# Kernel tuning notes

Measured on AMD Instinct MI355X. Metric: run time of the kernel, lower is better.

Reference implementation:

```python
import jax, jax.numpy as jnp
import numpy as np

B, T, DIM = 8, 2048, 512
DM, EXPAND, NSTATE, HDIM, L = 128, 2, 16, 64, 2
DINNER = DM * EXPAND            # 256
NH = DINNER // HDIM             # 4 heads
CONVDIM = DINNER + 2 * NSTATE   # 288 (n_groups=1)
PROJ = DINNER + CONVDIM + NH    # 548
K = 4                           # conv kernel (HF default)
EPS = 1e-5


def setup_inputs() -> dict:
    key = jax.random.key(0)
    ks = jax.random.split(key, 8)
    s = 0.02
    return {
        "x": jax.random.normal(ks[0], (B, T, DIM), jnp.float32),
        "in_w": jax.random.normal(ks[1], (DIM, DM), jnp.float32) * s,
        "in_b": jnp.zeros((DM,), jnp.float32),
        "norm_w": jnp.ones((L, DM), jnp.float32),
        "inproj_w": jax.random.normal(ks[2], (L, DM, PROJ), jnp.float32) * s,
        "conv_w": jax.random.normal(ks[3], (L, CONVDIM, 1, K), jnp.float32) * 0.2,
        "conv_b": jnp.zeros((L, CONVDIM), jnp.float32),
        "A_log": jnp.log(jax.random.uniform(ks[4], (L, NH), jnp.float32, 1.0, 8.0)),
        "D": jnp.ones((L, NH), jnp.float32),
        "dt_bias": jnp.log(jnp.expm1(jax.random.uniform(ks[5], (L, NH), jnp.float32, 1e-3, 0.1))),
        "gnorm_w": jnp.ones((L, DINNER), jnp.float32),
        "outproj_w": jax.random.normal(ks[6], (L, DINNER, DM), jnp.float32) * s,
        "normf_w": jnp.ones((DM,), jnp.float32),
        "out_w": jax.random.normal(ks[7], (DM, DIM), jnp.float32) * s,
        "out_b": jnp.zeros((DIM,), jnp.float32),
    }


def _rmsnorm(x, w):
    var = jnp.mean(x * x, axis=-1, keepdims=True)
    return x * jax.lax.rsqrt(var + EPS) * w


def _gated_rmsnorm(y, gate, w):
    y = y * jax.nn.silu(gate)
    var = jnp.mean(y * y, axis=-1, keepdims=True)
    return y * jax.lax.rsqrt(var + EPS) * w


def _causal_conv(h, w, b):
    # h: [B,T,C] depthwise causal conv, kernel K, left pad K-1
    out = jax.lax.conv_general_dilated(
        h.swapaxes(1, 2), w, (1,), [(K - 1, 0)],
        feature_group_count=CONVDIM,
        dimension_numbers=("NCH", "OIH", "NCH"))
    return out.swapaxes(1, 2) + b


def _ssd(xs, dt, A, Bm, Cm, Dh):
    # selective state-space scan (math-equivalent to HF Mamba2 chunked SSD)
    # xs [B,T,H,P], dt [B,T,H], A [H], Bm/Cm [B,T,N], Dh [H]
    dA = jnp.exp(dt * A)  # [B,T,H]

    def step(state, inp):
        dA_t, dt_t, x_t, B_t, C_t = inp
        dBx = dt_t[:, :, None, None] * x_t[..., None] * B_t[:, None, None, :]
        state = state * dA_t[:, :, None, None] + dBx  # [B,H,P,N]
        y = jnp.einsum("bhpn,bn->bhp", state, C_t)
        return state, y

    init = jnp.zeros((xs.shape[0], NH, HDIM, NSTATE), xs.dtype)
    _, ys = jax.lax.scan(step, init, (dA.swapaxes(0, 1), dt.swapaxes(0, 1),
                                      xs.swapaxes(0, 1), Bm.swapaxes(0, 1), Cm.swapaxes(0, 1)))
    return ys.swapaxes(0, 1) + xs * Dh[None, None, :, None]


def reference(x, in_w, in_b, norm_w, inproj_w, conv_w, conv_b, A_log, D,
              dt_bias, gnorm_w, outproj_w, normf_w, out_w, out_b):
    h = x @ in_w + in_b  # [B,T,DM]
    for l in range(L):
        res = h
        hn = _rmsnorm(h, norm_w[l])
        proj = hn @ inproj_w[l]  # [B,T,PROJ]
        gate = proj[..., :DINNER]
        hBC = proj[..., DINNER:DINNER + CONVDIM]
        dt = proj[..., DINNER + CONVDIM:]
        hBC = jax.nn.silu(_causal_conv(hBC, conv_w[l], conv_b[l]))
        xs = hBC[..., :DINNER].reshape(B, T, NH, HDIM)
        Bm = hBC[..., DINNER:DINNER + NSTATE]
        Cm = hBC[..., DINNER + NSTATE:]
        A = -jnp.exp(A_log[l])
        dt = jax.nn.softplus(dt + dt_bias[l])  # time_step_limit=(0,inf): no clamp
        y = _ssd(xs, dt, A, Bm, Cm, D[l]).reshape(B, T, DINNER)
        y = _gated_rmsnorm(y, gate, gnorm_w[l])
        h = res + y @ outproj_w[l]
    h = _rmsnorm(h, normf_w)
    pooled = h.mean(axis=1)  # mean pool over T
    return pooled @ out_w + out_b
```

## Files before the change

### kernel.cpp

```cpp
#include <hip/hip_runtime.h>
#include <math.h>

typedef unsigned short ushort_t;
typedef unsigned int uint_t;

#define B_      8
#define T_      2048
#define DIMX    512
#define DM      128
#define DINNER  256
#define NSTATE  16
#define HDIM    64
#define NH      4
#define CONVDIM 288
#define PROJ    548
#define KCONV   4
#define LLAYERS 2
#define QCH     128
#define NC      (T_/QCH)
#define EPSF    1e-5f
#define MTOK    (B_*T_)

#define OFF_H      0u
#define OFF_DTP    19988480u
#define OFF_CUM    20054016u
#define OFF_Z      20119552u
#define OFF_DEC    21168128u
#define OFF_PART   21168640u
#define OFF_WTIN   23396864u
#define OFF_WTINP  23429632u
#define OFF_WTOUT  23503360u
#define OFF_PROJB  23600000u
#define OFF_DTRAW  28100000u
#define OFF_HBCB   28200000u
#define OFF_YB     30600000u

__device__ __forceinline__ ushort_t f2b(float f) {
    uint_t u = __builtin_bit_cast(uint_t, f);
    return (ushort_t)((u + 0x7FFFu + ((u >> 16) & 1u)) >> 16);
}
__device__ __forceinline__ float b2f(ushort_t b) {
    uint_t u = ((uint_t)b) << 16;
    return __builtin_bit_cast(float, u);
}
__device__ __forceinline__ float blo(uint_t u) { return b2f((ushort_t)(u & 0xffffu)); }
__device__ __forceinline__ float bhi(uint_t u) { return b2f((ushort_t)(u >> 16)); }

typedef short bf8 __attribute__((ext_vector_type(8)));
typedef float f4v __attribute__((ext_vector_type(4)));

__global__ __launch_bounds__(256) void k_wt_all(
    const float* __restrict__ in_w, const float* __restrict__ inproj_w,
    const float* __restrict__ outproj_w,
    ushort_t* __restrict__ wt_in, ushort_t* __restrict__ wt_inp,
    ushort_t* __restrict__ wt_out)
{
    __shared__ float tile[64][65];
    int idx = blockIdx.x;
    const float* W; ushort_t* Wt; int K, N, k0, n0;
    if (idx < 16) {
        W = in_w; Wt = wt_in; K = 512; N = 128;
        k0 = (idx & 7) * 64; n0 = (idx >> 3) * 64;
    } else if (idx < 52) {
        int r = idx - 16; int l = r / 18; r -= l * 18;
        W = inproj_w + l * 128 * PROJ; Wt = wt_inp + l * 576 * 128; K = 128; N = PROJ;
        k0 = (r & 1) * 64; n0 = (r >> 1) * 64;
    } else {
        int r = idx - 52; int l = r / 8; r -= l * 8;
        W = outproj_w + l * 256 * 128; Wt = wt_out + l * 128 * 256; K = 256; N = 128;
        k0 = (r & 3) * 64; n0 = (r >> 2) * 64;
    }
    const int tid = threadIdx.x;
#pragma unroll
    for (int it = 0; it < 16; ++it) {
        const int e = it * 256 + tid;
        const int kk = e >> 6, nn = e & 63;
        tile[kk][nn] = (n0 + nn < N) ? W[(k0 + kk) * N + (n0 + nn)] : 0.f;
    }
    __syncthreads();
#pragma unroll
    for (int it = 0; it < 16; ++it) {
        const int e = it * 256 + tid;
        const int nn = e >> 6, kk = e & 63;
        Wt[(n0 + nn) * K + k0 + kk] = f2b(tile[kk][nn]);
    }
}

template<int KTOT, int LDC, int NGUARD, int EPI, bool ABF16>
__global__ __launch_bounds__(256) void k_gemm(
    const void* __restrict__ Ap, const ushort_t* __restrict__ Bt,
    const float* __restrict__ aux, float* __restrict__ C)
{
    __shared__ ushort_t Als[64 * 136];
    __shared__ ushort_t Bls[64 * 136];
    const int m0 = blockIdx.x * 64, n0 = blockIdx.y * 64;
    const int tid = threadIdx.x;
    const int lane = tid & 63, w = tid >> 6;
    const int wm = (w >> 1) * 32, wn = (w & 1) * 32;
    const int r16 = lane & 15, q8 = (lane >> 4) * 8;

    f4v acc[2][2];
#pragma unroll
    for (int i = 0; i < 2; ++i)
#pragma unroll
        for (int j = 0; j < 2; ++j) acc[i][j] = (f4v)0.f;

    for (int kc = 0; kc < KTOT; kc += 128) {
        if constexpr (ABF16) {
            const ushort_t* A = (const ushort_t*)Ap;
#pragma unroll
            for (int i = 0; i < 4; ++i) {
                const int e = i * 2048 + tid * 8;
                const int r = e >> 7, c = e & 127;
                *(uint4*)&Als[r * 136 + c] = *(const uint4*)&A[(m0 + r) * KTOT + kc + c];
            }
        } else {
            const float* A = (const float*)Ap;
#pragma unroll
            for (int i = 0; i < 4; ++i) {
                const int e = i * 2048 + tid * 8;
                const int r = e >> 7, c = e & 127;
                const float4 f0 = *(const float4*)&A[(m0 + r) * KTOT + kc + c];
                const float4 f1 = *(const float4*)&A[(m0 + r) * KTOT + kc + c + 4];
                uint4 pk;
                pk.x = (uint_t)f2b(f0.x) | ((uint_t)f2b(f0.y) << 16);
                pk.y = (uint_t)f2b(f0.z) | ((uint_t)f2b(f0.w) << 16);
                pk.z = (uint_t)f2b(f1.x) | ((uint_t)f2b(f1.y) << 16);
                pk.w = (uint_t)f2b(f1.z) | ((uint_t)f2b(f1.w) << 16);
                *(uint4*)&Als[r * 136 + c] = pk;
            }
        }
#pragma unroll
        for (int i = 0; i < 4; ++i) {
            const int e = i * 2048 + tid * 8;
            const int r = e >> 7, c = e & 127;
            *(uint4*)&Bls[r * 136 + c] = *(const uint4*)&Bt[(n0 + r) * KTOT + kc + c];
        }
        __syncthreads();
#pragma unroll
        for (int kk = 0; kk < 128; kk += 32) {
            const bf8 a0 = *(const bf8*)&Als[(wm + r16) * 136 + kk + q8];
            const bf8 a1 = *(const bf8*)&Als[(wm + 16 + r16) * 136 + kk + q8];
            const bf8 b0 = *(const bf8*)&Bls[(wn + r16) * 136 + kk + q8];
            const bf8 b1 = *(const bf8*)&Bls[(wn + 16 + r16) * 136 + kk + q8];
            acc[0][0] = __builtin_amdgcn_mfma_f32_16x16x32_bf16(a0, b0, acc[0][0], 0, 0, 0);
            acc[0][1] = __builtin_amdgcn_mfma_f32_16x16x32_bf16(a0, b1, acc[0][1], 0, 0, 0);
            acc[1][0] = __builtin_amdgcn_mfma_f32_16x16x32_bf16(a1, b0, acc[1][0], 0, 0, 0);
            acc[1][1] = __builtin_amdgcn_mfma_f32_16x16x32_bf16(a1, b1, acc[1][1], 0, 0, 0);
        }
        __syncthreads();
    }
    const int q4 = (lane >> 4) * 4;
#pragma unroll
    for (int i = 0; i < 2; ++i)
#pragma unroll
        for (int j = 0; j < 2; ++j)
#pragma unroll
            for (int r = 0; r < 4; ++r) {
                const int grow = m0 + wm + i * 16 + q4 + r;
                const int gcol = n0 + wn + j * 16 + r16;
                if (NGUARD == 0 || gcol < NGUARD) {
                    float v = acc[i][j][r];
                    if (EPI == 1) v += aux[gcol];
                    if (EPI == 2) v += C[grow * LDC + gcol];
                    C[grow * LDC + gcol] = v;
                }
            }
}

__global__ __launch_bounds__(256) void k_gemm_rms(
    const float* __restrict__ h, const float* __restrict__ nw,
    const ushort_t* __restrict__ Bt, ushort_t* __restrict__ projb,
    float* __restrict__ dtraw)
{
    __shared__ ushort_t Als[64 * 136];
    __shared__ ushort_t Bls[64 * 136];
    const int m0 = blockIdx.x * 64, n0 = blockIdx.y * 64;
    const int tid = threadIdx.x;
    const int lane = tid & 63, w = tid >> 6;
    const int wm = (w >> 1) * 32, wn = (w & 1) * 32;
    const int r16 = lane & 15, q8 = (lane >> 4) * 8;

#pragma unroll
    for (int i = 0; i < 4; ++i) {
        const int e = i * 2048 + tid * 8;
        const int r = e >> 7, c = e & 127;
        const float4 f0 = *(const float4*)&h[(m0 + r) * 128 + c];
        const float4 f1 = *(const float4*)&h[(m0 + r) * 128 + c + 4];
        float ss = f0.x * f0.x + f0.y * f0.y + f0.z * f0.z + f0.w * f0.w
                 + f1.x * f1.x + f1.y * f1.y + f1.z * f1.z + f1.w * f1.w;
#pragma unroll
        for (int off = 1; off < 16; off <<= 1) ss += __shfl_xor(ss, off);
        const float rs = rsqrtf(ss * (1.f / 128.f) + EPSF);
        const float4 w0 = *(const float4*)&nw[c];
        const float4 w1 = *(const float4*)&nw[c + 4];
        uint4 pk;
        pk.x = (uint_t)f2b(f0.x * rs * w0.x) | ((uint_t)f2b(f0.y * rs * w0.y) << 16);
        pk.y = (uint_t)f2b(f0.z * rs * w0.z) | ((uint_t)f2b(f0.w * rs * w0.w) << 16);
        pk.z = (uint_t)f2b(f1.x * rs * w1.x) | ((uint_t)f2b(f1.y * rs * w1.y) << 16);
        pk.w = (uint_t)f2b(f1.z * rs * w1.z) | ((uint_t)f2b(f1.w * rs * w1.w) << 16);
        *(uint4*)&Als[r * 136 + c] = pk;
    }
#pragma unroll
    for (int i = 0; i < 4; ++i) {
        const int e = i * 2048 + tid * 8;
        const int r = e >> 7, c = e & 127;
        *(uint4*)&Bls[r * 136 + c] = *(const uint4*)&Bt[(n0 + r) * 128 + c];
    }
    __syncthreads();

    f4v acc[2][2];
#pragma unroll
    for (int i = 0; i < 2; ++i)
#pragma unroll
        for (int j = 0; j < 2; ++j) acc[i][j] = (f4v)0.f;
#pragma unroll
    for (int kk = 0; kk < 128; kk += 32) {
        const bf8 a0 = *(const bf8*)&Als[(wm + r16) * 136 + kk + q8];
        const bf8 a1 = *(const bf8*)&Als[(wm + 16 + r16) * 136 + kk + q8];
        const bf8 b0 = *(const bf8*)&Bls[(wn + r16) * 136 + kk + q8];
        const bf8 b1 = *(const bf8*)&Bls[(wn + 16 + r16) * 136 + kk + q8];
        acc[0][0] = __builtin_amdgcn_mfma_f32_16x16x32_bf16(a0, b0, acc[0][0], 0, 0, 0);
        acc[0][1] = __builtin_amdgcn_mfma_f32_16x16x32_bf16(a0, b1, acc[0][1], 0, 0, 0);
        acc[1][0] = __builtin_amdgcn_mfma_f32_16x16x32_bf16(a1, b0, acc[1][0], 0, 0, 0);
        acc[1][1] = __builtin_amdgcn_mfma_f32_16x16x32_bf16(a1, b1, acc[1][1], 0, 0, 0);
    }

    const int q4 = (lane >> 4) * 4;
#pragma unroll
    for (int i = 0; i < 2; ++i)
#pragma unroll
        for (int j = 0; j < 2; ++j)
#pragma unroll
            for (int r = 0; r < 4; ++r) {
                const int grow = m0 + wm + i * 16 + q4 + r;
                const int gcol = n0 + wn + j * 16 + r16;
                if (gcol < 544) projb[grow * 544 + gcol] = f2b(acc[i][j][r]);
                else if (gcol < PROJ) dtraw[grow * 4 + (gcol - 544)] = acc[i][j][r];
            }
}

__global__ __launch_bounds__(256) void k_gemm_gn(
    const ushort_t* __restrict__ yb, const ushort_t* __restrict__ projb,
    const float* __restrict__ gw, const ushort_t* __restrict__ Bt,
    float* __restrict__ C)
{
    __shared__ ushort_t Als[64 * 264];
    __shared__ ushort_t Bls[64 * 136];
    const int m0 = blockIdx.x * 64, n0 = blockIdx.y * 64;
    const int tid = threadIdx.x;
    const int lane = tid & 63, w = tid >> 6;
    const int wm = (w >> 1) * 32, wn = (w & 1) * 32;
    const int r16 = lane & 15, q8 = (lane >> 4) * 8;

#pragma unroll
    for (int i = 0; i < 8; ++i) {
        const int e = i * 2048 + tid * 8;
        const int r = e >> 8, c = e & 255;
        const uint4 yv = *(const uint4*)&yb[(m0 + r) * 256 + c];
        const uint4 gv = *(const uint4*)&projb[(m0 + r) * 544 + c];
        const float g0 = blo(gv.x), g1 = bhi(gv.x), g2 = blo(gv.y), g3 = bhi(gv.y);
        const float g4 = blo(gv.z), g5 = bhi(gv.z), g6 = blo(gv.w), g7 = bhi(gv.w);
        float v0 = blo(yv.x) * (g0 / (1.f + __expf(-g0)));
        float v1 = bhi(yv.x) * (g1 / (1.f + __expf(-g1)));
        float v2 = blo(yv.y) * (g2 / (1.f + __expf(-g2)));
        float v3 = bhi(yv.y) * (g3 / (1.f + __expf(-g3)));
        float v4 = blo(yv.z) * (g4 / (1.f + __expf(-g4)));
        float v5 = bhi(yv.z) * (g5 / (1.f + __expf(-g5)));
        float v6 = blo(yv.w) * (g6 / (1.f + __expf(-g6)));
        float v7 = bhi(yv.w) * (g7 / (1.f + __expf(-g7)));
        float ss = v0 * v0 + v1 * v1 + v2 * v2 + v3 * v3
                 + v4 * v4 + v5 * v5 + v6 * v6 + v7 * v7;
#pragma unroll
        for (int off = 1; off < 32; off <<= 1) ss += __shfl_xor(ss, off);
        const float rs = rsqrtf(ss * (1.f / 256.f) + EPSF);
        const float4 w0 = *(const float4*)&gw[c];
        const float4 w1 = *(const float4*)&gw[c + 4];
        uint4 pk;
        pk.x = (uint_t)f2b(v0 * rs * w0.x) | ((uint_t)f2b(v1 * rs * w0.y) << 16);
        pk.y = (uint_t)f2b(v2 * rs * w0.z) | ((uint_t)f2b(v3 * rs * w0.w) << 16);
        pk.z = (uint_t)f2b(v4 * rs * w1.x) | ((uint_t)f2b(v5 * rs * w1.y) << 16);
        pk.w = (uint_t)f2b(v6 * rs * w1.z) | ((uint_t)f2b(v7 * rs * w1.w) << 16);
        *(uint4*)&Als[r * 264 + c] = pk;
    }

    f4v acc[2][2];
#pragma unroll
    for (int i = 0; i < 2; ++i)
#pragma unroll
        for (int j = 0; j < 2; ++j) acc[i][j] = (f4v)0.f;

    for (int kc = 0; kc < 256; kc += 128) {
#pragma unroll
        for (int i = 0; i < 4; ++i) {
            const int e = i * 2048 + tid * 8;
            const int r = e >> 7, c = e & 127;
            *(uint4*)&Bls[r * 136 + c] = *(const uint4*)&Bt[(n0 + r) * 256 + kc + c];
        }
        __syncthreads();
#pragma unroll
        for (int kk = 0; kk < 128; kk += 32) {
            const bf8 a0 = *(const bf8*)&Als[(wm + r16) * 264 + kc + kk + q8];
            const bf8 a1 = *(const bf8*)&Als[(wm + 16 + r16) * 264 + kc + kk + q8];
            const bf8 b0 = *(const bf8*)&Bls[(wn + r16) * 136 + kk + q8];
            const bf8 b1 = *(const bf8*)&Bls[(wn + 16 + r16) * 136 + kk + q8];
            acc[0][0] = __builtin_amdgcn_mfma_f32_16x16x32_bf16(a0, b0, acc[0][0], 0, 0, 0);
            acc[0][1] = __builtin_amdgcn_mfma_f32_16x16x32_bf16(a0, b1, acc[0][1], 0, 0, 0);
            acc[1][0] = __builtin_amdgcn_mfma_f32_16x16x32_bf16(a1, b0, acc[1][0], 0, 0, 0);
            acc[1][1] = __builtin_amdgcn_mfma_f32_16x16x32_bf16(a1, b1, acc[1][1], 0, 0, 0);
        }
        __syncthreads();
    }

    const int q4 = (lane >> 4) * 4;
#pragma unroll
    for (int i = 0; i < 2; ++i)
#pragma unroll
        for (int j = 0; j < 2; ++j)
#pragma unroll
            for (int r = 0; r < 4; ++r) {
                const int grow = m0 + wm + i * 16 + q4 + r;
                const int gcol = n0 + wn + j * 16 + r16;
                C[grow * 128 + gcol] += acc[i][j][r];
            }
}

__global__ __launch_bounds__(256) void k_convdt(
    const ushort_t* __restrict__ projb, const float* __restrict__ dtraw,
    const float* __restrict__ cw, const float* __restrict__ cb,
    const float* __restrict__ A_log, const float* __restrict__ dt_bias,
    ushort_t* __restrict__ hbcb, float* __restrict__ dtp,
    float* __restrict__ cum, int l)
{
    __shared__ float sc[128];
    const int bid = blockIdx.x;
    const int tid = threadIdx.x;
    if (bid < (MTOK * CONVDIM) / 256) {
        const int e = bid * 256 + tid;
        const int m = e / CONVDIM;
        const int cch = e - m * CONVDIM;
        const int b = m >> 11;
        const int t = m & (T_ - 1);
        const float* wp = cw + (l * CONVDIM + cch) * KCONV;
        float acc = cb[l * CONVDIM + cch];
#pragma unroll
        for (int k = 0; k < KCONV; ++k) {
            const int tt = t - (KCONV - 1) + k;
            if (tt >= 0) acc += b2f(projb[(b * T_ + tt) * 544 + 256 + cch]) * wp[k];
        }
        hbcb[m * CONVDIM + cch] = f2b(acc / (1.f + __expf(-acc)));
    } else {
        const int bid2 = bid - (MTOK * CONVDIM) / 256;
        const int c = bid2 & (NC - 1);
        const int hh = (bid2 / NC) & (NH - 1);
        const int b = bid2 / (NC * NH);
        const int t = tid;
        float dtv = 0.f;
        if (t < 128) {
            const int m = b * T_ + c * QCH + t;
            const float Ah = -expf(A_log[l * NH + hh]);
            const float raw = dtraw[m * 4 + hh] + dt_bias[l * NH + hh];
            dtv = (raw > 20.f) ? raw : log1pf(expf(raw));
            sc[t] = dtv * Ah;
        }
        __syncthreads();
        for (int off = 1; off < 128; off <<= 1) {
            const float v = (t >= off && t < 128) ? sc[t - off] : 0.f;
            __syncthreads();
            if (t < 128) sc[t] += v;
            __syncthreads();
        }
        if (t < 128) {
            const int m = b * T_ + c * QCH + t;
            dtp[m * NH + hh] = dtv;
            cum[m * NH + hh] = sc[t];
        }
    }
}

__global__ __launch_bounds__(256) void k_ssd_state(
    const ushort_t* __restrict__ hbcb, const float* __restrict__ dtp,
    const float* __restrict__ cum, float* __restrict__ zbuf,
    float* __restrict__ dec)
{
    __shared__ ushort_t Xt[64 * 136];
    __shared__ ushort_t wB[16 * 136];
    __shared__ float cumls[QCH];
    __shared__ float dtls[QCH];
    const int bid = blockIdx.x;
    const int c = bid & (NC - 1);
    const int hh = (bid / NC) & (NH - 1);
    const int b = bid / (NC * NH);
    const int m0 = b * T_ + c * QCH;
    const int tid = threadIdx.x;

    if (tid < QCH) {
        cumls[tid] = cum[(m0 + tid) * NH + hh];
        dtls[tid] = dtp[(m0 + tid) * NH + hh];
    }
    __syncthreads();
    const float clast = cumls[QCH - 1];
    {
        const int p = tid & 63;
        const int s0 = tid >> 6;
#pragma unroll
        for (int pass = 0; pass < 32; ++pass) {
            const int s = s0 + pass * 4;
            Xt[p * 136 + s] = hbcb[(m0 + s) * CONVDIM + hh * 64 + p];
        }
    }
    for (int e = tid; e < QCH * 16; e += 256) {
        const int n = e & 15, s = e >> 4;
        const float w = __expf(clast - cumls[s]) * dtls[s];
        wB[n * 136 + s] = f2b(w * b2f(hbcb[(m0 + s) * CONVDIM + DINNER + n]));
    }
    __syncthreads();

    const int lane = tid & 63, w = tid >> 6;
    const int r16 = lane & 15, q8 = (lane >> 4) * 8, q4 = (lane >> 4) * 4;
    f4v acc = (f4v)0.f;
#pragma unroll
    for (int kc = 0; kc < 128; kc += 32) {
        const bf8 a = *(const bf8*)&Xt[(w * 16 + r16) * 136 + kc + q8];
        const bf8 bb = *(const bf8*)&wB[r16 * 136 + kc + q8];
        acc = __builtin_amdgcn_mfma_f32_16x16x32_bf16(a, bb, acc, 0, 0, 0);
    }
#pragma unroll
    for (int r = 0; r < 4; ++r) {
        const int p = w * 16 + q4 + r;
        zbuf[bid * 1024 + p * 16 + r16] = acc[r];
    }
    if (tid == 0) dec[bid] = __expf(clast);
}

__global__ __launch_bounds__(256) void k_ssd_y(
    const ushort_t* __restrict__ hbcb, const float* __restrict__ dtp,
    const float* __restrict__ cum, const float* __restrict__ zbuf,
    const float* __restrict__ dec, const float* __restrict__ Dvec,
    ushort_t* __restrict__ yb, int l)
{
    __shared__ ushort_t Xt[64 * 136];
    __shared__ ushort_t BlsT[128 * 40];
    __shared__ ushort_t ClsT[128 * 40];
    __shared__ ushort_t Gls[128 * 136];
    __shared__ ushort_t Spt[64 * 40];
    __shared__ float cumls[QCH];
    __shared__ float dtls[QCH];
    const int bid = blockIdx.x;
    const int c = bid & (NC - 1);
    const int hh = (bid / NC) & (NH - 1);
    const int b = bid / (NC * NH);
    const int bh = bid >> 4;
    const int m0 = b * T_ + c * QCH;
    const int tid = threadIdx.x;

    if (tid < QCH) {
        cumls[tid] = cum[(m0 + tid) * NH + hh];
        dtls[tid] = dtp[(m0 + tid) * NH + hh];
    }
    {
        const int p = tid & 63;
        const int s0 = tid >> 6;
#pragma unroll
        for (int pass = 0; pass < 32; ++pass) {
            const int s = s0 + pass * 4;
            Xt[p * 136 + s] = hbcb[(m0 + s) * CONVDIM + hh * 64 + p];
        }
    }
    for (int e = tid; e < QCH * 16; e += 256) {
        const int n = e & 15, s = e >> 4;
        BlsT[s * 40 + n] = hbcb[(m0 + s) * CONVDIM + DINNER + n];
        BlsT[s * 40 + 16 + n] = 0;
        ClsT[s * 40 + n] = hbcb[(m0 + s) * CONVDIM + DINNER + NSTATE + n];
        ClsT[s * 40 + 16 + n] = 0;
    }
    {
        float4 S; S.x = 0.f; S.y = 0.f; S.z = 0.f; S.w = 0.f;
        for (int cc = 0; cc < c; ++cc) {
            const float d = dec[bh * NC + cc];
            const float4 z = *(const float4*)(zbuf + (bh * NC + cc) * 1024 + tid * 4);
            S.x = S.x * d + z.x; S.y = S.y * d + z.y;
            S.z = S.z * d + z.z; S.w = S.w * d + z.w;
        }
        const int p = tid >> 2, n = (tid & 3) * 4;
        Spt[p * 40 + n]     = f2b(S.x);
        Spt[p * 40 + n + 1] = f2b(S.y);
        Spt[p * 40 + n + 2] = f2b(S.z);
        Spt[p * 40 + n + 3] = f2b(S.w);
        Spt[p * 40 + 16 + n]     = 0;
        Spt[p * 40 + 16 + n + 1] = 0;
        Spt[p * 40 + 16 + n + 2] = 0;
        Spt[p * 40 + 16 + n + 3] = 0;
    }
    __syncthreads();

    const int lane = tid & 63, w = tid >> 6;
    const int wrow = w * 32;
    const int r16 = lane & 15, q8 = (lane >> 4) * 8, q4 = (lane >> 4) * 4;
    const float Dh = Dvec[l * NH + hh];

    bf8 cfr[2];
#pragma unroll
    for (int i = 0; i < 2; ++i)
        cfr[i] = *(const bf8*)&ClsT[(wrow + i * 16 + r16) * 40 + q8];

    float cumt[8], et[8];
#pragma unroll
    for (int i = 0; i < 2; ++i)
#pragma unroll
        for (int r = 0; r < 4; ++r) {
            const int t = wrow + i * 16 + q4 + r;
            cumt[i * 4 + r] = cumls[t];
            et[i * 4 + r] = __expf(cumls[t]);
        }

    f4v acc[2][4];
#pragma unroll
    for (int j = 0; j < 4; ++j) {
        const bf8 sf = *(const bf8*)&Spt[(j * 16 + r16) * 40 + q8];
#pragma unroll
        for (int i = 0; i < 2; ++i) {
            f4v z = (f4v)0.f;
            z = __builtin_amdgcn_mfma_f32_16x16x32_bf16(cfr[i], sf, z, 0, 0, 0);
#pragma unroll
            for (int r = 0; r < 4; ++r) {
                const int t = wrow + i * 16 + q4 + r;
                const int p = j * 16 + r16;
                acc[i][j][r] = z[r] * et[i * 4 + r] + Dh * b2f(Xt[p * 136 + t]);
            }
        }
    }

#pragma unroll
    for (int ts = 0; ts < 8; ++ts) {
        const bf8 bf = *(const bf8*)&BlsT[(ts * 16 + r16) * 40 + q8];
        const int s = ts * 16 + r16;
        const float cs = cumls[s];
        const float ds = dtls[s];
#pragma unroll
        for (int i = 0; i < 2; ++i) {
            f4v g = (f4v)0.f;
            g = __builtin_amdgcn_mfma_f32_16x16x32_bf16(cfr[i], bf, g, 0, 0, 0);
#pragma unroll
            for (int r = 0; r < 4; ++r) {
                const int t = wrow + i * 16 + q4 + r;
                const float val = (s <= t) ? __expf(cumt[i * 4 + r] - cs) * ds * g[r] : 0.f;
                Gls[t * 136 + s] = f2b(val);
            }
        }
    }
    __syncthreads();

#pragma unroll
    for (int kc = 0; kc < 128; kc += 32) {
        bf8 af[2];
#pragma unroll
        for (int i = 0; i < 2; ++i)
            af[i] = *(const bf8*)&Gls[(wrow + i * 16 + r16) * 136 + kc + q8];
#pragma unroll
        for (int j = 0; j < 4; ++j) {
            const bf8 xf = *(const bf8*)&Xt[(j * 16 + r16) * 136 + kc + q8];
#pragma unroll
            for (int i = 0; i < 2; ++i)
                acc[i][j] = __builtin_amdgcn_mfma_f32_16x16x32_bf16(af[i], xf, acc[i][j], 0, 0, 0);
        }
    }

#pragma unroll
    for (int i = 0; i < 2; ++i)
#pragma unroll
        for (int r = 0; r < 4; ++r) {
            const int t = wrow + i * 16 + q4 + r;
#pragma unroll
            for (int j = 0; j < 4; ++j) {
                const int p = j * 16 + r16;
                yb[(m0 + t) * DINNER + hh * 64 + p] = f2b(acc[i][j][r]);
            }
        }
}

__global__ __launch_bounds__(256) void k_finalnorm_pool(
    const float* __restrict__ h, const float* __restrict__ nfw,
    float* __restrict__ part)
{
    __shared__ float ht[2048];
    __shared__ float red[256];
    __shared__ float rstd[16];
    __shared__ float padd[256];
    const int tile = blockIdx.x & 127;
    const int b = blockIdx.x >> 7;
    const int m0 = b * T_ + tile * 16;
    const int tid = threadIdx.x;
    for (int e = tid; e < 2048; e += 256) ht[e] = h[m0 * DM + e];
    __syncthreads();
    {
        const int tg = tid >> 4, j0 = tid & 15;
        float p = 0.f;
#pragma unroll
        for (int k = 0; k < 8; ++k) { const float v = ht[tg * 128 + j0 + 16 * k]; p += v * v; }
        red[tid] = p;
    }
    __syncthreads();
    if (tid < 16) {
        float s = 0.f;
#pragma unroll
        for (int q = 0; q < 16; ++q) s += red[tid * 16 + q];
        rstd[tid] = rsqrtf(s * (1.f / 128.f) + EPSF);
    }
    __syncthreads();
    const int d = tid & 127, half = tid >> 7;
    float ps = 0.f;
#pragma unroll
    for (int i0 = 0; i0 < 8; ++i0) { const int i = half + 2 * i0; ps += ht[i * 128 + d] * rstd[i]; }
    padd[tid] = ps;
    __syncthreads();
    if (tid < 128) part[(b * 128 + tile) * 128 + tid] = (padd[tid] + padd[128 + tid]) * nfw[tid];
}

__global__ __launch_bounds__(256) void k_head(
    const float* __restrict__ part, const float* __restrict__ ow,
    const float* __restrict__ ob, float* __restrict__ out)
{
    __shared__ float pooled[128];
    const int b = blockIdx.x;
    const int tid = threadIdx.x;
    if (tid < 128) {
        float s = 0.f;
        for (int tile = 0; tile < 128; ++tile) s += part[(b * 128 + tile) * 128 + tid];
        pooled[tid] = s * (1.f / (float)T_);
    }
    __syncthreads();
    for (int o = tid; o < DIMX; o += 256) {
        float acc = ob[o];
#pragma unroll 4
        for (int d = 0; d < 128; ++d) acc += pooled[d] * ow[d * DIMX + o];
        out[b * DIMX + o] = acc;
    }
}

extern "C" void kernel_launch(void* const* d_in, const int* in_sizes, int n_in,
                              void* d_out, int out_size, void* d_ws, size_t ws_size,
                              hipStream_t stream)
{
    const float* x         = (const float*)d_in[0];
    const float* in_w      = (const float*)d_in[1];
    const float* in_b      = (const float*)d_in[2];
    const float* norm_w    = (const float*)d_in[3];
    const float* inproj_w  = (const float*)d_in[4];
    const float* conv_w    = (const float*)d_in[5];
    const float* conv_b    = (const float*)d_in[6];
    const float* A_log     = (const float*)d_in[7];
    const float* Dvec      = (const float*)d_in[8];
    const float* dt_bias   = (const float*)d_in[9];
    const float* gnorm_w   = (const float*)d_in[10];
    const float* outproj_w = (const float*)d_in[11];
    const float* normf_w   = (const float*)d_in[12];
    const float* out_w     = (const float*)d_in[13];
    const float* out_b     = (const float*)d_in[14];

    float* ws    = (float*)d_ws;
    float* h     = ws + OFF_H;
    float* dtp   = ws + OFF_DTP;
    float* cumb  = ws + OFF_CUM;
    float* zbuf  = ws + OFF_Z;
    float* dec   = ws + OFF_DEC;
    float* part  = ws + OFF_PART;
    float* dtraw = ws + OFF_DTRAW;
    ushort_t* projb = (ushort_t*)(ws + OFF_PROJB);
    ushort_t* hbcb  = (ushort_t*)(ws + OFF_HBCB);
    ushort_t* yb    = (ushort_t*)(ws + OFF_YB);
    ushort_t* wt_in  = (ushort_t*)(ws + OFF_WTIN);
    ushort_t* wt_inp = (ushort_t*)(ws + OFF_WTINP);
    ushort_t* wt_out = (ushort_t*)(ws + OFF_WTOUT);

    k_wt_all<<<68, 256, 0, stream>>>(in_w, inproj_w, outproj_w, wt_in, wt_inp, wt_out);

    k_gemm<512, 128, 0, 1, false><<<dim3(MTOK / 64, 2), 256, 0, stream>>>(x, wt_in, in_b, h);

    for (int l = 0; l < LLAYERS; ++l) {
        k_gemm_rms<<<dim3(MTOK / 64, 9), 256, 0, stream>>>(
            h, norm_w + l * DM, wt_inp + l * 576 * 128, projb, dtraw);
        k_convdt<<<(MTOK * CONVDIM) / 256 + B_ * NH * NC, 256, 0, stream>>>(
            projb, dtraw, conv_w, conv_b, A_log, dt_bias, hbcb, dtp, cumb, l);
        k_ssd_state<<<B_ * NH * NC, 256, 0, stream>>>(hbcb, dtp, cumb, zbuf, dec);
        k_ssd_y<<<B_ * NH * NC, 256, 0, stream>>>(hbcb, dtp, cumb, zbuf, dec, Dvec, yb, l);
        k_gemm_gn<<<dim3(MTOK / 64, 2), 256, 0, stream>>>(
            yb, projb, gnorm_w + l * DINNER, wt_out + l * 128 * 256, h);
    }

    k_finalnorm_pool<<<B_ * (T_ / 16), 256, 0, stream>>>(h, normf_w, part);
    k_head<<<B_, 256, 0, stream>>>(part, out_w, out_b, (float*)d_out);
}
```

Baseline: 277.4 us.

## Widen in-proj GEMM N-tile to 128 and vectorize SSD shared-memory staging loads

The RMSNorm+in-projection GEMM now computes 64x128 output tiles, with each wave covering 64 columns. This cuts the grid from 9 to 5 column blocks, so the normalized A tile is recomputed fewer times, and rows past 576 are zero-padded. The SSD state and output kernels now stage X, B and C from global memory with 16-byte uint4 loads and unpack them into the transposed LDS tiles, replacing scalar 2-byte gathers. The trade-offs are higher register and LDS use in the GEMM and some wasted compute on the padded last tile.

```diff
diff --git a/kernel.cpp b/kernel.cpp
--- a/kernel.cpp
+++ b/kernel.cpp
@@ -174,11 +174,11 @@
     float* __restrict__ dtraw)
 {
     __shared__ ushort_t Als[64 * 136];
-    __shared__ ushort_t Bls[64 * 136];
-    const int m0 = blockIdx.x * 64, n0 = blockIdx.y * 64;
+    __shared__ ushort_t Bls[128 * 136];
+    const int m0 = blockIdx.x * 64, n0 = blockIdx.y * 128;
     const int tid = threadIdx.x;
     const int lane = tid & 63, w = tid >> 6;
-    const int wm = (w >> 1) * 32, wn = (w & 1) * 32;
+    const int wm = (w >> 1) * 32, wn = (w & 1) * 64;
     const int r16 = lane & 15, q8 = (lane >> 4) * 8;
 
 #pragma unroll
@@ -202,35 +202,38 @@
         *(uint4*)&Als[r * 136 + c] = pk;
     }
 #pragma unroll
-    for (int i = 0; i < 4; ++i) {
+    for (int i = 0; i < 8; ++i) {
         const int e = i * 2048 + tid * 8;
         const int r = e >> 7, c = e & 127;
-        *(uint4*)&Bls[r * 136 + c] = *(const uint4*)&Bt[(n0 + r) * 128 + c];
-    }
-    __syncthreads();
-
-    f4v acc[2][2];
-#pragma unroll
-    for (int i = 0; i < 2; ++i)
-#pragma unroll
-        for (int j = 0; j < 2; ++j) acc[i][j] = (f4v)0.f;
+        const int row = n0 + r;
+        uint4 v; v.x = 0u; v.y = 0u; v.z = 0u; v.w = 0u;
+        if (row < 576) v = *(const uint4*)&Bt[row * 128 + c];
+        *(uint4*)&Bls[r * 136 + c] = v;
+    }
+    __syncthreads();
+
+    f4v acc[2][4];
+#pragma unroll
+    for (int i = 0; i < 2; ++i)
+#pragma unroll
+        for (int j = 0; j < 4; ++j) acc[i][j] = (f4v)0.f;
 #pragma unroll
     for (int kk = 0; kk < 128; kk += 32) {
         const bf8 a0 = *(const bf8*)&Als[(wm + r16) * 136 + kk + q8];
         const bf8 a1 = *(const bf8*)&Als[(wm + 16 + r16) * 136 + kk + q8];
-        const bf8 b0 = *(const bf8*)&Bls[(wn + r16) * 136 + kk + q8];
-        const bf8 b1 = *(const bf8*)&Bls[(wn + 16 + r16) * 136 + kk + q8];
-        acc[0][0] = __builtin_amdgcn_mfma_f32_16x16x32_bf16(a0, b0, acc[0][0], 0, 0, 0);
-        acc[0][1] = __builtin_amdgcn_mfma_f32_16x16x32_bf16(a0, b1, acc[0][1], 0, 0, 0);
-        acc[1][0] = __builtin_amdgcn_mfma_f32_16x16x32_bf16(a1, b0, acc[1][0], 0, 0, 0);
-        acc[1][1] = __builtin_amdgcn_mfma_f32_16x16x32_bf16(a1, b1, acc[1][1], 0, 0, 0);
+#pragma unroll
+        for (int j = 0; j < 4; ++j) {
+            const bf8 bj = *(const bf8*)&Bls[(wn + j * 16 + r16) * 136 + kk + q8];
+            acc[0][j] = __builtin_amdgcn_mfma_f32_16x16x32_bf16(a0, bj, acc[0][j], 0, 0, 0);
+            acc[1][j] = __builtin_amdgcn_mfma_f32_16x16x32_bf16(a1, bj, acc[1][j], 0, 0, 0);
+        }
     }
 
     const int q4 = (lane >> 4) * 4;
 #pragma unroll
     for (int i = 0; i < 2; ++i)
 #pragma unroll
-        for (int j = 0; j < 2; ++j)
+        for (int j = 0; j < 4; ++j)
 #pragma unroll
             for (int r = 0; r < 4; ++r) {
                 const int grow = m0 + wm + i * 16 + q4 + r;
@@ -401,18 +404,31 @@
     __syncthreads();
     const float clast = cumls[QCH - 1];
     {
-        const int p = tid & 63;
-        const int s0 = tid >> 6;
-#pragma unroll
-        for (int pass = 0; pass < 32; ++pass) {
-            const int s = s0 + pass * 4;
-            Xt[p * 136 + s] = hbcb[(m0 + s) * CONVDIM + hh * 64 + p];
-        }
-    }
-    for (int e = tid; e < QCH * 16; e += 256) {
-        const int n = e & 15, s = e >> 4;
+        const int sl = tid >> 3;
+        const int p0 = (tid & 7) * 8;
+#pragma unroll
+        for (int pass = 0; pass < 4; ++pass) {
+            const int s = pass * 32 + sl;
+            const uint4 v = *(const uint4*)&hbcb[(m0 + s) * CONVDIM + hh * 64 + p0];
+            const uint_t vv[4] = {v.x, v.y, v.z, v.w};
+#pragma unroll
+            for (int k = 0; k < 4; ++k) {
+                Xt[(p0 + 2 * k) * 136 + s]     = (ushort_t)(vv[k] & 0xffffu);
+                Xt[(p0 + 2 * k + 1) * 136 + s] = (ushort_t)(vv[k] >> 16);
+            }
+        }
+    }
+    {
+        const int s = tid >> 1;
+        const int nq = (tid & 1) * 8;
+        const uint4 v = *(const uint4*)&hbcb[(m0 + s) * CONVDIM + DINNER + nq];
         const float w = __expf(clast - cumls[s]) * dtls[s];
-        wB[n * 136 + s] = f2b(w * b2f(hbcb[(m0 + s) * CONVDIM + DINNER + n]));
+        const uint_t vv[4] = {v.x, v.y, v.z, v.w};
+#pragma unroll
+        for (int k = 0; k < 4; ++k) {
+            wB[(nq + 2 * k) * 136 + s]     = f2b(w * blo(vv[k]));
+            wB[(nq + 2 * k + 1) * 136 + s] = f2b(w * bhi(vv[k]));
+        }
     }
     __syncthreads();
 
@@ -459,20 +475,40 @@
         dtls[tid] = dtp[(m0 + tid) * NH + hh];
     }
     {
-        const int p = tid & 63;
-        const int s0 = tid >> 6;
-#pragma unroll
-        for (int pass = 0; pass < 32; ++pass) {
-            const int s = s0 + pass * 4;
-            Xt[p * 136 + s] = hbcb[(m0 + s) * CONVDIM + hh * 64 + p];
-        }
-    }
-    for (int e = tid; e < QCH * 16; e += 256) {
-        const int n = e & 15, s = e >> 4;
-        BlsT[s * 40 + n] = hbcb[(m0 + s) * CONVDIM + DINNER + n];
-        BlsT[s * 40 + 16 + n] = 0;
-        ClsT[s * 40 + n] = hbcb[(m0 + s) * CONVDIM + DINNER + NSTATE + n];
-        ClsT[s * 40 + 16 + n] = 0;
+        const int sl = tid >> 3;
+        const int p0 = (tid & 7) * 8;
+#pragma unroll
+        for (int pass = 0; pass < 4; ++pass) {
+            const int s = pass * 32 + sl;
+            const uint4 v = *(const uint4*)&hbcb[(m0 + s) * CONVDIM + hh * 64 + p0];
+            const uint_t vv[4] = {v.x, v.y, v.z, v.w};
+#pragma unroll
+            for (int k = 0; k < 4; ++k) {
+                Xt[(p0 + 2 * k) * 136 + s]     = (ushort_t)(vv[k] & 0xffffu);
+                Xt[(p0 + 2 * k + 1) * 136 + s] = (ushort_t)(vv[k] >> 16);
+            }
+        }
+    }
+    {
+#pragma unroll
+        for (int pass = 0; pass < 2; ++pass) {
+            const int task = pass * 256 + tid;
+            const int s = task >> 2, q = task & 3;
+            const uint4 v = *(const uint4*)&hbcb[(m0 + s) * CONVDIM + DINNER + q * 8];
+            const uint_t vv[4] = {v.x, v.y, v.z, v.w};
+            ushort_t* dst = (q < 2) ? &BlsT[s * 40 + (q & 1) * 8]
+                                    : &ClsT[s * 40 + (q & 1) * 8];
+#pragma unroll
+            for (int k = 0; k < 4; ++k) {
+                dst[2 * k]     = (ushort_t)(vv[k] & 0xffffu);
+                dst[2 * k + 1] = (ushort_t)(vv[k] >> 16);
+            }
+        }
+        for (int e = tid; e < 2048; e += 256) {
+            const int s = e >> 4, n = e & 15;
+            BlsT[s * 40 + 16 + n] = 0;
+            ClsT[s * 40 + 16 + n] = 0;
+        }
     }
     {
         float4 S; S.x = 0.f; S.y = 0.f; S.z = 0.f; S.w = 0.f;
@@ -678,7 +714,7 @@
     k_gemm<512, 128, 0, 1, false><<<dim3(MTOK / 64, 2), 256, 0, stream>>>(x, wt_in, in_b, h);
 
     for (int l = 0; l < LLAYERS; ++l) {
-        k_gemm_rms<<<dim3(MTOK / 64, 9), 256, 0, stream>>>(
+        k_gemm_rms<<<dim3(MTOK / 64, 5), 256, 0, stream>>>(
             h, norm_w + l * DM, wt_inp + l * 576 * 128, projb, dtraw);
         k_convdt<<<(MTOK * CONVDIM) / 256 + B_ * NH * NC, 256, 0, stream>>>(
             projb, dtraw, conv_w, conv_b, A_log, dt_bias, hbcb, dtp, cumb, l);
```

Measured after the change: 282.0 us. Within noise of the previous version (+1.7%).

## Fuse causal conv and dt cumsum into SSD state and output kernels

Applied to the files above, without the earlier changes.

Removes the separate conv/dt kernel and its hbcb/dtp/cum intermediate buffers. Each SSD kernel now loads the raw projection rows for its chunk, plus a 3-step halo, into shared memory and computes the depthwise conv, SiLU, softplus dt and chunk-local cumsum itself. This saves a launch and a global write and read of the conv output, at the cost of doing the conv and scan twice (once per SSD kernel) and using more shared memory.

```diff
diff --git a/kernel.cpp b/kernel.cpp
--- a/kernel.cpp
+++ b/kernel.cpp
@@ -22,8 +22,6 @@
 #define MTOK    (B_*T_)
 
 #define OFF_H      0u
-#define OFF_DTP    19988480u
-#define OFF_CUM    20054016u
 #define OFF_Z      20119552u
 #define OFF_DEC    21168128u
 #define OFF_PART   21168640u
@@ -32,7 +30,6 @@
 #define OFF_WTOUT  23503360u
 #define OFF_PROJB  23600000u
 #define OFF_DTRAW  28100000u
-#define OFF_HBCB   28200000u
 #define OFF_YB     30600000u
 
 __device__ __forceinline__ ushort_t f2b(float f) {
@@ -325,68 +322,19 @@
             }
 }
 
-__global__ __launch_bounds__(256) void k_convdt(
+__global__ __launch_bounds__(256) void k_ssd_state(
     const ushort_t* __restrict__ projb, const float* __restrict__ dtraw,
     const float* __restrict__ cw, const float* __restrict__ cb,
     const float* __restrict__ A_log, const float* __restrict__ dt_bias,
-    ushort_t* __restrict__ hbcb, float* __restrict__ dtp,
-    float* __restrict__ cum, int l)
-{
-    __shared__ float sc[128];
-    const int bid = blockIdx.x;
-    const int tid = threadIdx.x;
-    if (bid < (MTOK * CONVDIM) / 256) {
-        const int e = bid * 256 + tid;
-        const int m = e / CONVDIM;
-        const int cch = e - m * CONVDIM;
-        const int b = m >> 11;
-        const int t = m & (T_ - 1);
-        const float* wp = cw + (l * CONVDIM + cch) * KCONV;
-        float acc = cb[l * CONVDIM + cch];
-#pragma unroll
-        for (int k = 0; k < KCONV; ++k) {
-            const int tt = t - (KCONV - 1) + k;
-            if (tt >= 0) acc += b2f(projb[(b * T_ + tt) * 544 + 256 + cch]) * wp[k];
-        }
-        hbcb[m * CONVDIM + cch] = f2b(acc / (1.f + __expf(-acc)));
-    } else {
-        const int bid2 = bid - (MTOK * CONVDIM) / 256;
-        const int c = bid2 & (NC - 1);
-        const int hh = (bid2 / NC) & (NH - 1);
-        const int b = bid2 / (NC * NH);
-        const int t = tid;
-        float dtv = 0.f;
-        if (t < 128) {
-            const int m = b * T_ + c * QCH + t;
-            const float Ah = -expf(A_log[l * NH + hh]);
-            const float raw = dtraw[m * 4 + hh] + dt_bias[l * NH + hh];
-            dtv = (raw > 20.f) ? raw : log1pf(expf(raw));
-            sc[t] = dtv * Ah;
-        }
-        __syncthreads();
-        for (int off = 1; off < 128; off <<= 1) {
-            const float v = (t >= off && t < 128) ? sc[t - off] : 0.f;
-            __syncthreads();
-            if (t < 128) sc[t] += v;
-            __syncthreads();
-        }
-        if (t < 128) {
-            const int m = b * T_ + c * QCH + t;
-            dtp[m * NH + hh] = dtv;
-            cum[m * NH + hh] = sc[t];
-        }
-    }
-}
-
-__global__ __launch_bounds__(256) void k_ssd_state(
-    const ushort_t* __restrict__ hbcb, const float* __restrict__ dtp,
-    const float* __restrict__ cum, float* __restrict__ zbuf,
-    float* __restrict__ dec)
+    float* __restrict__ zbuf, float* __restrict__ dec, int l)
 {
     __shared__ ushort_t Xt[64 * 136];
     __shared__ ushort_t wB[16 * 136];
+    __shared__ ushort_t pX[131 * 64];
+    __shared__ ushort_t pB[131 * 16];
     __shared__ float cumls[QCH];
     __shared__ float dtls[QCH];
+    __shared__ float sc[QCH];
     const int bid = blockIdx.x;
     const int c = bid & (NC - 1);
     const int hh = (bid / NC) & (NH - 1);
@@ -394,25 +342,71 @@
     const int m0 = b * T_ + c * QCH;
     const int tid = threadIdx.x;
 
-    if (tid < QCH) {
-        cumls[tid] = cum[(m0 + tid) * NH + hh];
-        dtls[tid] = dtp[(m0 + tid) * NH + hh];
+    float dtv = 0.f;
+    if (tid < 128) {
+        const float Ah = -expf(A_log[l * NH + hh]);
+        const float raw = dtraw[(m0 + tid) * 4 + hh] + dt_bias[l * NH + hh];
+        dtv = (raw > 20.f) ? raw : log1pf(expf(raw));
+        sc[tid] = dtv * Ah;
+    }
+    __syncthreads();
+    for (int off = 1; off < 128; off <<= 1) {
+        const float v = (tid >= off && tid < 128) ? sc[tid - off] : 0.f;
+        __syncthreads();
+        if (tid < 128) sc[tid] += v;
+        __syncthreads();
+    }
+    if (tid < 128) { dtls[tid] = dtv; cumls[tid] = sc[tid]; }
+
+    {
+        const int t0 = c * QCH;
+        for (int e = tid; e < 131 * 8; e += 256) {
+            const int ls = e >> 3, j = e & 7;
+            const int tb = t0 + ls - 3;
+            uint4 v; v.x = 0u; v.y = 0u; v.z = 0u; v.w = 0u;
+            if (tb >= 0) v = *(const uint4*)&projb[(b * T_ + tb) * 544 + 256 + hh * 64 + j * 8];
+            *(uint4*)&pX[ls * 64 + j * 8] = v;
+        }
+        for (int e = tid; e < 131 * 2; e += 256) {
+            const int ls = e >> 1, j = e & 1;
+            const int tb = t0 + ls - 3;
+            uint4 v; v.x = 0u; v.y = 0u; v.z = 0u; v.w = 0u;
+            if (tb >= 0) v = *(const uint4*)&projb[(b * T_ + tb) * 544 + 512 + j * 8];
+            *(uint4*)&pB[ls * 16 + j * 8] = v;
+        }
     }
     __syncthreads();
     const float clast = cumls[QCH - 1];
+
     {
         const int p = tid & 63;
         const int s0 = tid >> 6;
+        const float* wp = cw + (l * CONVDIM + hh * 64 + p) * KCONV;
+        const float bbv = cb[l * CONVDIM + hh * 64 + p];
 #pragma unroll
         for (int pass = 0; pass < 32; ++pass) {
-            const int s = s0 + pass * 4;
-            Xt[p * 136 + s] = hbcb[(m0 + s) * CONVDIM + hh * 64 + p];
-        }
-    }
-    for (int e = tid; e < QCH * 16; e += 256) {
-        const int n = e & 15, s = e >> 4;
-        const float w = __expf(clast - cumls[s]) * dtls[s];
-        wB[n * 136 + s] = f2b(w * b2f(hbcb[(m0 + s) * CONVDIM + DINNER + n]));
+            const int s = pass * 4 + s0;
+            float a = bbv;
+#pragma unroll
+            for (int k = 0; k < KCONV; ++k) a += b2f(pX[(s + k) * 64 + p]) * wp[k];
+            Xt[p * 136 + s] = f2b(a / (1.f + __expf(-a)));
+        }
+    }
+    {
+        const int n = tid & 15;
+        const int s0 = tid >> 4;
+        const float* wp = cw + (l * CONVDIM + 256 + n) * KCONV;
+        const float bbv = cb[l * CONVDIM + 256 + n];
+#pragma unroll
+        for (int pass = 0; pass < 8; ++pass) {
+            const int s = pass * 16 + s0;
+            float a = bbv;
+#pragma unroll
+            for (int k = 0; k < KCONV; ++k) a += b2f(pB[(s + k) * 16 + n]) * wp[k];
+            const ushort_t sb = f2b(a / (1.f + __expf(-a)));
+            const float w = __expf(clast - cumls[s]) * dtls[s];
+            wB[n * 136 + s] = f2b(w * b2f(sb));
+        }
     }
     __syncthreads();
 
@@ -434,10 +428,11 @@
 }
 
 __global__ __launch_bounds__(256) void k_ssd_y(
-    const ushort_t* __restrict__ hbcb, const float* __restrict__ dtp,
-    const float* __restrict__ cum, const float* __restrict__ zbuf,
-    const float* __restrict__ dec, const float* __restrict__ Dvec,
-    ushort_t* __restrict__ yb, int l)
+    const ushort_t* __restrict__ projb, const float* __restrict__ dtraw,
+    const float* __restrict__ cw, const float* __restrict__ cb,
+    const float* __restrict__ A_log, const float* __restrict__ dt_bias,
+    const float* __restrict__ zbuf, const float* __restrict__ dec,
+    const float* __restrict__ Dvec, ushort_t* __restrict__ yb, int l)
 {
     __shared__ ushort_t Xt[64 * 136];
     __shared__ ushort_t BlsT[128 * 40];
@@ -446,6 +441,10 @@
     __shared__ ushort_t Spt[64 * 40];
     __shared__ float cumls[QCH];
     __shared__ float dtls[QCH];
+    __shared__ float sc[QCH];
+    ushort_t* pX = Gls;
+    ushort_t* pB = Gls + 131 * 64;
+    ushort_t* pC = Gls + 131 * 64 + 131 * 16;
     const int bid = blockIdx.x;
     const int c = bid & (NC - 1);
     const int hh = (bid / NC) & (NH - 1);
@@ -454,25 +453,82 @@
     const int m0 = b * T_ + c * QCH;
     const int tid = threadIdx.x;
 
-    if (tid < QCH) {
-        cumls[tid] = cum[(m0 + tid) * NH + hh];
-        dtls[tid] = dtp[(m0 + tid) * NH + hh];
-    }
+    float dtv = 0.f;
+    if (tid < 128) {
+        const float Ah = -expf(A_log[l * NH + hh]);
+        const float raw = dtraw[(m0 + tid) * 4 + hh] + dt_bias[l * NH + hh];
+        dtv = (raw > 20.f) ? raw : log1pf(expf(raw));
+        sc[tid] = dtv * Ah;
+    }
+    __syncthreads();
+    for (int off = 1; off < 128; off <<= 1) {
+        const float v = (tid >= off && tid < 128) ? sc[tid - off] : 0.f;
+        __syncthreads();
+        if (tid < 128) sc[tid] += v;
+        __syncthreads();
+    }
+    if (tid < 128) { dtls[tid] = dtv; cumls[tid] = sc[tid]; }
+
+    {
+        const int t0 = c * QCH;
+        for (int e = tid; e < 131 * 8; e += 256) {
+            const int ls = e >> 3, j = e & 7;
+            const int tb = t0 + ls - 3;
+            uint4 v; v.x = 0u; v.y = 0u; v.z = 0u; v.w = 0u;
+            if (tb >= 0) v = *(const uint4*)&projb[(b * T_ + tb) * 544 + 256 + hh * 64 + j * 8];
+            *(uint4*)&pX[ls * 64 + j * 8] = v;
+        }
+        for (int e = tid; e < 131 * 2; e += 256) {
+            const int ls = e >> 1, j = e & 1;
+            const int tb = t0 + ls - 3;
+            uint4 v0; v0.x = 0u; v0.y = 0u; v0.z = 0u; v0.w = 0u;
+            uint4 v1 = v0;
+            if (tb >= 0) {
+                v0 = *(const uint4*)&projb[(b * T_ + tb) * 544 + 512 + j * 8];
+                v1 = *(const uint4*)&projb[(b * T_ + tb) * 544 + 528 + j * 8];
+            }
+            *(uint4*)&pB[ls * 16 + j * 8] = v0;
+            *(uint4*)&pC[ls * 16 + j * 8] = v1;
+        }
+    }
+    __syncthreads();
+    const float clast_unused = cumls[QCH - 1]; (void)clast_unused;
+
     {
         const int p = tid & 63;
         const int s0 = tid >> 6;
+        const float* wp = cw + (l * CONVDIM + hh * 64 + p) * KCONV;
+        const float bbv = cb[l * CONVDIM + hh * 64 + p];
 #pragma unroll
         for (int pass = 0; pass < 32; ++pass) {
-            const int s = s0 + pass * 4;
-            Xt[p * 136 + s] = hbcb[(m0 + s) * CONVDIM + hh * 64 + p];
-        }
-    }
-    for (int e = tid; e < QCH * 16; e += 256) {
-        const int n = e & 15, s = e >> 4;
-        BlsT[s * 40 + n] = hbcb[(m0 + s) * CONVDIM + DINNER + n];
-        BlsT[s * 40 + 16 + n] = 0;
-        ClsT[s * 40 + n] = hbcb[(m0 + s) * CONVDIM + DINNER + NSTATE + n];
-        ClsT[s * 40 + 16 + n] = 0;
+            const int s = pass * 4 + s0;
+            float a = bbv;
+#pragma unroll
+            for (int k = 0; k < KCONV; ++k) a += b2f(pX[(s + k) * 64 + p]) * wp[k];
+            Xt[p * 136 + s] = f2b(a / (1.f + __expf(-a)));
+        }
+    }
+    {
+        const int n = tid & 15;
+        const int s0 = tid >> 4;
+        const float* wpB = cw + (l * CONVDIM + 256 + n) * KCONV;
+        const float bbB = cb[l * CONVDIM + 256 + n];
+        const float* wpC = cw + (l * CONVDIM + 272 + n) * KCONV;
+        const float bbC = cb[l * CONVDIM + 272 + n];
+#pragma unroll
+        for (int pass = 0; pass < 8; ++pass) {
+            const int s = pass * 16 + s0;
+            float aB = bbB, aC = bbC;
+#pragma unroll
+            for (int k = 0; k < KCONV; ++k) {
+                aB += b2f(pB[(s + k) * 16 + n]) * wpB[k];
+                aC += b2f(pC[(s + k) * 16 + n]) * wpC[k];
+            }
+            BlsT[s * 40 + n] = f2b(aB / (1.f + __expf(-aB)));
+            ClsT[s * 40 + n] = f2b(aC / (1.f + __expf(-aC)));
+            BlsT[s * 40 + 16 + n] = 0;
+            ClsT[s * 40 + 16 + n] = 0;
+        }
     }
     {
         float4 S; S.x = 0.f; S.y = 0.f; S.z = 0.f; S.w = 0.f;
@@ -660,14 +716,11 @@
 
     float* ws    = (float*)d_ws;
     float* h     = ws + OFF_H;
-    float* dtp   = ws + OFF_DTP;
-    float* cumb  = ws + OFF_CUM;
     float* zbuf  = ws + OFF_Z;
     float* dec   = ws + OFF_DEC;
     float* part  = ws + OFF_PART;
     float* dtraw = ws + OFF_DTRAW;
     ushort_t* projb = (ushort_t*)(ws + OFF_PROJB);
-    ushort_t* hbcb  = (ushort_t*)(ws + OFF_HBCB);
     ushort_t* yb    = (ushort_t*)(ws + OFF_YB);
     ushort_t* wt_in  = (ushort_t*)(ws + OFF_WTIN);
     ushort_t* wt_inp = (ushort_t*)(ws + OFF_WTINP);
@@ -680,10 +733,10 @@
     for (int l = 0; l < LLAYERS; ++l) {
         k_gemm_rms<<<dim3(MTOK / 64, 9), 256, 0, stream>>>(
             h, norm_w + l * DM, wt_inp + l * 576 * 128, projb, dtraw);
-        k_convdt<<<(MTOK * CONVDIM) / 256 + B_ * NH * NC, 256, 0, stream>>>(
-            projb, dtraw, conv_w, conv_b, A_log, dt_bias, hbcb, dtp, cumb, l);
-        k_ssd_state<<<B_ * NH * NC, 256, 0, stream>>>(hbcb, dtp, cumb, zbuf, dec);
-        k_ssd_y<<<B_ * NH * NC, 256, 0, stream>>>(hbcb, dtp, cumb, zbuf, dec, Dvec, yb, l);
+        k_ssd_state<<<B_ * NH * NC, 256, 0, stream>>>(
+            projb, dtraw, conv_w, conv_b, A_log, dt_bias, zbuf, dec, l);
+        k_ssd_y<<<B_ * NH * NC, 256, 0, stream>>>(
+            projb, dtraw, conv_w, conv_b, A_log, dt_bias, zbuf, dec, Dvec, yb, l);
         k_gemm_gn<<<dim3(MTOK / 64, 2), 256, 0, stream>>>(
             yb, projb, gnorm_w + l * DINNER, wt_out + l * 128 * 256, h);
     }
```

Measured after the change: 253.2 us. -8.7%, faster.
